# Optimization experiments

Measured on AMD Instinct MI355X. Metric: run time of the kernel, lower is better.

Reference implementation:

```python
import jax, jax.numpy as jnp
import numpy as np

NEG_SLOPE = 0.2
HEADS = 8

def _gat_conv(x, src, dst, n_nodes, W, att_src, att_dst, bias):
    # x: [N, Fin], W: [Fin, H*C], att_*: [H, C], bias: [C]
    H, C = att_src.shape
    xl = (x @ W).reshape(n_nodes, H, C)                      # [N,H,C]
    a_src = (xl * att_src[None]).sum(-1)                      # [N,H]
    a_dst = (xl * att_dst[None]).sum(-1)                      # [N,H]
    e = jax.nn.leaky_relu(a_src[src] + a_dst[dst], NEG_SLOPE) # [E,H]
    m = jax.ops.segment_max(e, dst, num_segments=n_nodes)     # [N,H]
    ee = jnp.exp(e - m[dst])
    s = jax.ops.segment_sum(ee, dst, num_segments=n_nodes)    # [N,H]
    alpha = ee / s[dst]                                       # [E,H]
    msg = alpha[:, :, None] * xl[src]                         # [E,H,C]
    out = jax.ops.segment_sum(msg, dst, num_segments=n_nodes) # [N,H,C]
    return out.mean(axis=1) + bias                            # [N,C] (concat=False)

def setup_inputs() -> dict:
    key = jax.random.key(0)
    ks = jax.random.split(key, 12)
    N, E, EL = 50000, 800000, 200000
    V, D, HID, OUT = 5000, 128, 32, 32
    inp = {}
    inp['x'] = jax.random.randint(ks[0], (N,), 0, V)
    inp['edge_index'] = jax.random.randint(ks[1], (2, E), 0, N)
    inp['edge_label_index'] = jax.random.randint(ks[2], (2, EL), 0, N)
    inp['emb'] = jax.random.normal(ks[3], (V, D), jnp.float32) * D ** -0.5
    inp['W1'] = jax.random.normal(ks[4], (D, HEADS * HID), jnp.float32) * D ** -0.5
    inp['att_src1'] = jax.random.normal(ks[5], (HEADS, HID), jnp.float32) * HID ** -0.5
    inp['att_dst1'] = jax.random.normal(ks[6], (HEADS, HID), jnp.float32) * HID ** -0.5
    inp['b1'] = jnp.zeros((HID,), jnp.float32)
    inp['W2'] = jax.random.normal(ks[7], (HID, HEADS * OUT), jnp.float32) * HID ** -0.5
    inp['att_src2'] = jax.random.normal(ks[8], (HEADS, OUT), jnp.float32) * OUT ** -0.5
    inp['att_dst2'] = jax.random.normal(ks[9], (HEADS, OUT), jnp.float32) * OUT ** -0.5
    inp['b2'] = jnp.zeros((OUT,), jnp.float32)
    return inp

def reference(x, edge_index, edge_label_index, emb, W1, att_src1, att_dst1, b1, W2, att_src2, att_dst2, b2):
    N = x.shape[0]
    # PyG GATConv adds self-loops by default
    loop = jnp.arange(N)
    src = jnp.concatenate([edge_index[0], loop])
    dst = jnp.concatenate([edge_index[1], loop])
    h = emb[x]                                                   # [N, D] embedding lookup (squeeze(1) equivalent)
    h = jax.nn.relu(_gat_conv(h, src, dst, N, W1, att_src1, att_dst1, b1))
    # dropout p=0.5 is identity at inference (training=False)
    z = _gat_conv(h, src, dst, N, W2, att_src2, att_dst2, b2)    # [N, OUT]
    # decode: dot product over label edges
    return (z[edge_label_index[0]] * z[edge_label_index[1]]).sum(axis=-1)
```

## Files before the change

### kernel.cpp

```cpp
#include <hip/hip_runtime.h>
#include <hip/hip_fp16.h>
#include <math.h>
#include <limits.h>

#define HH 8
#define CC 32
#define NEG 0.2f

struct __align__(8) half4 { __half2 a, b; };
typedef float f32x4 __attribute__((ext_vector_type(4)));

__device__ __forceinline__ int ldnt(const int* p){ return __builtin_nontemporal_load(p); }
__device__ __forceinline__ float ldntf(const float* p){ return __builtin_nontemporal_load(p); }
__device__ __forceinline__ f32x4 ldnt4(const float* p){ return __builtin_nontemporal_load((const f32x4*)p); }
__device__ __forceinline__ void stnt4(float* p, f32x4 v){ __builtin_nontemporal_store(v, (f32x4*)p); }
__device__ __forceinline__ int f2ord(float f){ int i=__float_as_int(f); return i>=0? i : i^0x7fffffff; }
__device__ __forceinline__ float ord2f(int i){ return __int_as_float(i>=0? i : i^0x7fffffff); }

__device__ __forceinline__ void edge_sd_nt(const int* __restrict__ ei, int e, int E, int& s, int& d){
  if(e < E){ s = ldnt(ei+e); d = ldnt(ei+E+e); } else { s = e-E; d = s; }
}

__global__ void k_init2(int* __restrict__ cnt, int* __restrict__ gmax, int N){
  int i = blockIdx.x*blockDim.x + threadIdx.x;
  if(i < N) cnt[i] = 0;
  if(i < 16) gmax[i] = INT_MIN;
}

__global__ void k_count(const int* __restrict__ ei, int E, int ET, int* __restrict__ cnt){
  int e = blockIdx.x*blockDim.x + threadIdx.x;
  if(e >= ET) return;
  int d = (e < E) ? ldnt(ei+E+e) : e-E;
  atomicAdd(&cnt[d], 1);
}

__global__ __launch_bounds__(256) void k_scan_block(const int* __restrict__ cnt,
                                                    int* __restrict__ off,
                                                    int* __restrict__ bsum, int N){
  int i = blockIdx.x*256 + threadIdx.x;
  int v = (i < N) ? cnt[i] : 0;
  int lane = threadIdx.x & 63;
  int incl = v;
  #pragma unroll
  for(int o=1;o<64;o<<=1){ int u = __shfl_up(incl,o); if(lane>=o) incl += u; }
  __shared__ int wsum[4];
  if(lane==63) wsum[threadIdx.x>>6] = incl;
  __syncthreads();
  int w = threadIdx.x>>6, wadd = 0;
  #pragma unroll
  for(int k=0;k<4;k++) if(k<w) wadd += wsum[k];
  if(i < N) off[i] = wadd + incl - v;
  if(threadIdx.x==255) bsum[blockIdx.x] = wadd + incl;
}

__global__ __launch_bounds__(256) void k_scan_bsum(int* __restrict__ bsum, int nb,
                                                   int* __restrict__ offN){
  int t = threadIdx.x;
  int v = (t < nb) ? bsum[t] : 0;
  int lane = t & 63;
  int incl = v;
  #pragma unroll
  for(int o=1;o<64;o<<=1){ int u = __shfl_up(incl,o); if(lane>=o) incl += u; }
  __shared__ int wsum[4];
  if(lane==63) wsum[t>>6] = incl;
  __syncthreads();
  int w = t>>6, wadd = 0;
  #pragma unroll
  for(int k=0;k<4;k++) if(k<w) wadd += wsum[k];
  if(t < nb) bsum[t] = wadd + incl - v;
  if(t == 255) *offN = wadd + incl;
}

__global__ void k_scan_add(int* __restrict__ off, const int* __restrict__ bsum,
                           int* __restrict__ cur, int N){
  int i = blockIdx.x*256 + threadIdx.x;
  if(i < N){ int v = off[i] + bsum[blockIdx.x]; off[i] = v; cur[i] = v; }
}

__global__ void k_scatter(const int* __restrict__ ei, int E, int ET,
                          const int* __restrict__ x,
                          int* __restrict__ cur, int* __restrict__ csr_src,
                          int* __restrict__ csr_xv){
  int e = blockIdx.x*blockDim.x + threadIdx.x;
  if(e >= ET) return;
  int s,d; edge_sd_nt(ei,e,E,s,d);
  int pos = atomicAdd(&cur[d], 1);
  csr_src[pos] = s;
  csr_xv[pos]  = x[s];
}

__global__ __launch_bounds__(256) void k_ws(const float* __restrict__ W2,
                                            const float* __restrict__ att_s2,
                                            const float* __restrict__ att_d2,
                                            float* __restrict__ ws_s, float* __restrict__ ws_d){
  int k = threadIdx.x >> 3, h = threadIdx.x & 7;
  float ss = 0.f, dd = 0.f;
  for(int c=0;c<CC;c++){
    float w = W2[k*256 + h*CC + c];
    ss = fmaf(w, att_s2[h*CC+c], ss);
    dd = fmaf(w, att_d2[h*CC+c], dd);
  }
  ws_s[k*HH+h] = ss;
  ws_d[k*HH+h] = dd;
}

__global__ __launch_bounds__(256) void k_gmax(const float* __restrict__ a, int n8,
                                              int* __restrict__ gmax){
  int tid = blockIdx.x*256 + threadIdx.x;
  int lane = threadIdx.x & 63;
  float m = -INFINITY;
  for(int i = tid; i < n8; i += gridDim.x*256) m = fmaxf(m, a[i]);
  #pragma unroll
  for(int msk=8; msk<64; msk<<=1) m = fmaxf(m, __shfl_xor(m, msk));
  if(lane < 8) atomicMax(&gmax[lane], f2ord(m));
}

__global__ __launch_bounds__(256,4) void k_gemm1(
    const float* __restrict__ X, const float* __restrict__ W,
    const float* __restrict__ att_s, const float* __restrict__ att_d,
    __half* __restrict__ xl, float* __restrict__ a_src, float* __restrict__ a_dst,
    int* __restrict__ gmax1, int V){
  const int ROWS = 8, FIN = 128;
  __shared__ __align__(16) float xs[ROWS][FIN];
  __shared__ int smax[8];
  int row0 = blockIdx.x*ROWS;
  int tid = threadIdx.x;
  if(tid < 8) smax[tid] = INT_MIN;
  for(int p = tid; p < ROWS*FIN; p += 256){
    int r = p/FIN, kk = p - r*FIN;
    int row = row0 + r;
    xs[r][kk] = (row < V) ? ldntf(X + (size_t)row*FIN + kk) : 0.f;
  }
  __syncthreads();
  float acc[ROWS];
  #pragma unroll
  for(int r=0;r<ROWS;r++) acc[r]=0.f;
  for(int k=0;k<FIN;k++){
    float w = W[(size_t)k*256 + tid];
    #pragma unroll
    for(int r=0;r<ROWS;r++) acc[r] = fmaf(xs[r][k], w, acc[r]);
  }
  float as = att_s[tid], ad = att_d[tid];
  #pragma unroll
  for(int r=0;r<ROWS;r++){
    int n = row0+r;
    float v = acc[r];
    float ps = v*as, pd = v*ad;
    #pragma unroll
    for(int msk=16; msk>=1; msk>>=1){
      ps += __shfl_xor(ps, msk);
      pd += __shfl_xor(pd, msk);
    }
    if(n < V){
      xl[(size_t)n*256 + tid] = __float2half(v);
      if((tid&31)==0){
        int hh = tid>>5;
        a_src[n*HH+hh] = ps;
        a_dst[n*HH+hh] = pd;
        atomicMax(&smax[hh], f2ord(ps));
      }
    }
  }
  __syncthreads();
  if(tid < 8) atomicMax(&gmax1[tid], smax[tid]);
}

__global__ __launch_bounds__(256) void k_fused1(
    const int* __restrict__ off, const int* __restrict__ csr_xv,
    const int* __restrict__ x,
    const float* __restrict__ a_src_v, const float* __restrict__ a_dst_v,
    const int* __restrict__ gmax1,
    const __half* __restrict__ xl_v, const float* __restrict__ bias,
    const float* __restrict__ ws_s, const float* __restrict__ ws_d,
    __half* __restrict__ h2h, float* __restrict__ a_src2, float* __restrict__ a_dst2, int N){
  int wid = (int)((blockIdx.x*(size_t)blockDim.x + threadIdx.x) >> 6);
  int lane = threadIdx.x & 63;
  if(wid >= N) return;
  const int start = off[wid], end = off[wid+1];
  const int t = lane >> 3, h = lane & 7;
  const int xv_n = x[wid];
  const float ad = a_dst_v[xv_n*HH + h];
  float mb = ord2f(gmax1[h]) + ad;
  mb = mb > 0.f ? mb : NEG*mb;

  const int h2 = lane >> 3, c0 = (lane & 7)*4;
  const __half* xp = xl_v + h2*CC + c0;

  int sv = ldnt(csr_xv + min(start + t, end-1));
  float sraw = a_src_v[sv*HH + h] + ad;
  bool valid = (start + t) < end;

  float eesum = 0.f;
  float4 acc = make_float4(0.f,0.f,0.f,0.f);
  for(int j0 = start; j0 < end; j0 += 8){
    int svn = 0; float srawn = 0.f; bool validn = false;
    if(j0 + 8 < end){
      int jjn = j0 + 8 + t;
      svn = ldnt(csr_xv + min(jjn, end-1));
      srawn = a_src_v[svn*HH + h] + ad;
      validn = jjn < end;
    }
    float v = sraw > 0.f ? sraw : NEG*sraw;
    float ee = valid ? __expf(v - mb) : 0.f;
    eesum += ee;
    float av[8];
    #pragma unroll
    for(int u=0;u<8;u++) av[u] = __shfl(ee, u*8 + h2);
    int s0 = __builtin_amdgcn_readlane(sv, 0);
    int s1 = __builtin_amdgcn_readlane(sv, 8);
    int s2 = __builtin_amdgcn_readlane(sv, 16);
    int s3 = __builtin_amdgcn_readlane(sv, 24);
    int s4 = __builtin_amdgcn_readlane(sv, 32);
    int s5 = __builtin_amdgcn_readlane(sv, 40);
    int s6 = __builtin_amdgcn_readlane(sv, 48);
    int s7 = __builtin_amdgcn_readlane(sv, 56);
    uint2 rv[8];
    rv[0] = *reinterpret_cast<const uint2*>(xp + (size_t)s0*256);
    rv[1] = *reinterpret_cast<const uint2*>(xp + (size_t)s1*256);
    rv[2] = *reinterpret_cast<const uint2*>(xp + (size_t)s2*256);
    rv[3] = *reinterpret_cast<const uint2*>(xp + (size_t)s3*256);
    rv[4] = *reinterpret_cast<const uint2*>(xp + (size_t)s4*256);
    rv[5] = *reinterpret_cast<const uint2*>(xp + (size_t)s5*256);
    rv[6] = *reinterpret_cast<const uint2*>(xp + (size_t)s6*256);
    rv[7] = *reinterpret_cast<const uint2*>(xp + (size_t)s7*256);
    #pragma unroll
    for(int u=0;u<8;u++){
      __half2 ha = *reinterpret_cast<__half2*>(&rv[u].x);
      __half2 hb = *reinterpret_cast<__half2*>(&rv[u].y);
      float2 f01 = __half22float2(ha), f23 = __half22float2(hb);
      acc.x = fmaf(av[u], f01.x, acc.x);
      acc.y = fmaf(av[u], f01.y, acc.y);
      acc.z = fmaf(av[u], f23.x, acc.z);
      acc.w = fmaf(av[u], f23.y, acc.w);
    }
    sv = svn; sraw = srawn; valid = validn;
  }
  #pragma unroll
  for(int msk=8; msk<64; msk<<=1) eesum += __shfl_xor(eesum, msk);
  float is2 = 0.125f / __shfl(eesum, h2);
  acc.x *= is2; acc.y *= is2; acc.z *= is2; acc.w *= is2;
  #pragma unroll
  for(int msk=8; msk<64; msk<<=1){
    acc.x += __shfl_xor(acc.x, msk);
    acc.y += __shfl_xor(acc.y, msk);
    acc.z += __shfl_xor(acc.z, msk);
    acc.w += __shfl_xor(acc.w, msk);
  }
  if(lane < 8){
    const float4 b = *reinterpret_cast<const float4*>(bias + c0);
    float4 o = make_float4(fmaxf(acc.x+b.x,0.f), fmaxf(acc.y+b.y,0.f),
                           fmaxf(acc.z+b.z,0.f), fmaxf(acc.w+b.w,0.f));
    half4 hv;
    hv.a = __floats2half2_rn(o.x, o.y);
    hv.b = __floats2half2_rn(o.z, o.w);
    *reinterpret_cast<half4*>(h2h + (size_t)wid*CC + c0) = hv;
    float ps = 0.f, pd = 0.f;
    #pragma unroll
    for(int g=0; g<8; ++g){
      float v0 = __shfl(o.x, g), v1 = __shfl(o.y, g), v2 = __shfl(o.z, g), v3 = __shfl(o.w, g);
      int kb = g*4;
      ps = fmaf(v0, ws_s[(kb+0)*HH+lane], ps);
      ps = fmaf(v1, ws_s[(kb+1)*HH+lane], ps);
      ps = fmaf(v2, ws_s[(kb+2)*HH+lane], ps);
      ps = fmaf(v3, ws_s[(kb+3)*HH+lane], ps);
      pd = fmaf(v0, ws_d[(kb+0)*HH+lane], pd);
      pd = fmaf(v1, ws_d[(kb+1)*HH+lane], pd);
      pd = fmaf(v2, ws_d[(kb+2)*HH+lane], pd);
      pd = fmaf(v3, ws_d[(kb+3)*HH+lane], pd);
    }
    a_src2[wid*HH + lane] = ps;
    a_dst2[wid*HH + lane] = pd;
  }
}

__global__ __launch_bounds__(256) void k_agg2(
    const int* __restrict__ off, const int* __restrict__ csr_src,
    const float* __restrict__ a_src2, const float* __restrict__ a_dst2,
    const int* __restrict__ gmax2,
    const __half* __restrict__ h2h, float* __restrict__ agg, int N){
  int wid = (int)((blockIdx.x*(size_t)blockDim.x + threadIdx.x) >> 6);
  int lane = threadIdx.x & 63;
  if(wid >= N) return;
  const int start = off[wid], end = off[wid+1];
  const int t = lane >> 3, h = lane & 7;
  const float ad = a_dst2[wid*HH + h];
  float mb = ord2f(gmax2[h]) + ad;
  mb = mb > 0.f ? mb : NEG*mb;

  const int h2 = lane >> 3, k0 = (lane & 7)*4;
  const __half* hp = h2h + k0;

  int sv = ldnt(csr_src + min(start + t, end-1));
  float sraw = a_src2[sv*HH + h] + ad;
  bool valid = (start + t) < end;

  float eesum = 0.f;
  float4 acc = make_float4(0.f,0.f,0.f,0.f);
  for(int j0 = start; j0 < end; j0 += 8){
    int svn = 0; float srawn = 0.f; bool validn = false;
    if(j0 + 8 < end){
      int jjn = j0 + 8 + t;
      svn = ldnt(csr_src + min(jjn, end-1));
      srawn = a_src2[svn*HH + h] + ad;
      validn = jjn < end;
    }
    float v = sraw > 0.f ? sraw : NEG*sraw;
    float ee = valid ? __expf(v - mb) : 0.f;
    eesum += ee;
    float av[8];
    #pragma unroll
    for(int u=0;u<8;u++) av[u] = __shfl(ee, u*8 + h2);
    int s0 = __builtin_amdgcn_readlane(sv, 0);
    int s1 = __builtin_amdgcn_readlane(sv, 8);
    int s2 = __builtin_amdgcn_readlane(sv, 16);
    int s3 = __builtin_amdgcn_readlane(sv, 24);
    int s4 = __builtin_amdgcn_readlane(sv, 32);
    int s5 = __builtin_amdgcn_readlane(sv, 40);
    int s6 = __builtin_amdgcn_readlane(sv, 48);
    int s7 = __builtin_amdgcn_readlane(sv, 56);
    uint2 rv[8];
    rv[0] = *reinterpret_cast<const uint2*>(hp + (size_t)s0*CC);
    rv[1] = *reinterpret_cast<const uint2*>(hp + (size_t)s1*CC);
    rv[2] = *reinterpret_cast<const uint2*>(hp + (size_t)s2*CC);
    rv[3] = *reinterpret_cast<const uint2*>(hp + (size_t)s3*CC);
    rv[4] = *reinterpret_cast<const uint2*>(hp + (size_t)s4*CC);
    rv[5] = *reinterpret_cast<const uint2*>(hp + (size_t)s5*CC);
    rv[6] = *reinterpret_cast<const uint2*>(hp + (size_t)s6*CC);
    rv[7] = *reinterpret_cast<const uint2*>(hp + (size_t)s7*CC);
    #pragma unroll
    for(int u=0;u<8;u++){
      __half2 ha = *reinterpret_cast<__half2*>(&rv[u].x);
      __half2 hb = *reinterpret_cast<__half2*>(&rv[u].y);
      float2 f01 = __half22float2(ha), f23 = __half22float2(hb);
      acc.x = fmaf(av[u], f01.x, acc.x);
      acc.y = fmaf(av[u], f01.y, acc.y);
      acc.z = fmaf(av[u], f23.x, acc.z);
      acc.w = fmaf(av[u], f23.y, acc.w);
    }
    sv = svn; sraw = srawn; valid = validn;
  }
  #pragma unroll
  for(int msk=8; msk<64; msk<<=1) eesum += __shfl_xor(eesum, msk);
  float is2 = 0.125f / __shfl(eesum, h2);
  f32x4 o; o.x = acc.x*is2; o.y = acc.y*is2; o.z = acc.z*is2; o.w = acc.w*is2;
  stnt4(agg + (size_t)wid*256 + lane*4, o);
}

__global__ __launch_bounds__(256) void k_trans2(
    const float* __restrict__ agg, const float* __restrict__ W2,
    const float* __restrict__ b2, float* __restrict__ z, int N){
  __shared__ __align__(16) float aggl[4][256];
  int w = threadIdx.x >> 6, lane = threadIdx.x & 63;
  int wid = (int)(blockIdx.x*4 + w);
  bool active = wid < N;
  f32x4 av = {0.f,0.f,0.f,0.f};
  if(active) av = ldnt4(agg + (size_t)wid*256 + lane*4);
  *reinterpret_cast<f32x4*>(&aggl[w][lane*4]) = av;
  __syncthreads();

  const int ch = lane & 31, part = lane >> 5;
  float p0=0.f, p1=0.f, p2=0.f, p3=0.f;
  #pragma unroll
  for(int hh = 0; hh < 4; ++hh){
    int hq = part*4 + hh;
    const float* wcol = W2 + hq*CC + ch;
    const float* a = &aggl[w][hq*CC];
    #pragma unroll
    for(int k=0;k<CC;k+=4){
      p0 = fmaf(a[k+0], wcol[(size_t)(k+0)*256], p0);
      p1 = fmaf(a[k+1], wcol[(size_t)(k+1)*256], p1);
      p2 = fmaf(a[k+2], wcol[(size_t)(k+2)*256], p2);
      p3 = fmaf(a[k+3], wcol[(size_t)(k+3)*256], p3);
    }
  }
  float p = (p0+p1)+(p2+p3);
  p += __shfl_xor(p, 32);
  if(active && part==0) z[(size_t)wid*CC + ch] = p + b2[ch];
}

__global__ void k_decode(const int* __restrict__ eli, int EL,
                         const float* __restrict__ z, float* __restrict__ out){
  int e = blockIdx.x*blockDim.x + threadIdx.x;
  if(e >= EL) return;
  const float4* za = reinterpret_cast<const float4*>(z + (size_t)ldnt(eli+e)*CC);
  const float4* zb = reinterpret_cast<const float4*>(z + (size_t)ldnt(eli+EL+e)*CC);
  float s = 0.f;
  #pragma unroll
  for(int j=0;j<8;j++){
    float4 u = za[j], v = zb[j];
    s += u.x*v.x + u.y*v.y + u.z*v.z + u.w*v.w;
  }
  out[e] = s;
}

extern "C" void kernel_launch(void* const* d_in, const int* in_sizes, int n_in,
                              void* d_out, int out_size, void* d_ws, size_t ws_size,
                              hipStream_t stream){
  const int*   x   = (const int*)d_in[0];
  const int*   ei  = (const int*)d_in[1];
  const int*   eli = (const int*)d_in[2];
  const float* emb = (const float*)d_in[3];
  const float* W1  = (const float*)d_in[4];
  const float* as1 = (const float*)d_in[5];
  const float* ad1 = (const float*)d_in[6];
  const float* b1  = (const float*)d_in[7];
  const float* W2  = (const float*)d_in[8];
  const float* as2 = (const float*)d_in[9];
  const float* ad2 = (const float*)d_in[10];
  const float* b2  = (const float*)d_in[11];

  const int N  = in_sizes[0];
  const int V  = in_sizes[3]/128;
  const int E  = in_sizes[1]/2;
  const int EL = in_sizes[2]/2;
  const int ET = E + N;

  __half* xl_v = (__half*)d_ws;
  __half* h2h  = xl_v + (size_t)V*256;
  float* a_src_v = (float*)(h2h + (size_t)N*CC);
  float* a_dst_v = a_src_v + (size_t)V*HH;
  float* a_src2  = a_dst_v + (size_t)V*HH;
  float* a_dst2  = a_src2 + (size_t)N*HH;
  float* z       = a_dst2 + (size_t)N*HH;
  float* agg     = z + (size_t)N*CC;
  float* ws_s    = agg + (size_t)N*256;
  float* ws_d    = ws_s + 256;
  int*   gmax1   = (int*)(ws_d + 256);
  int*   gmax2   = gmax1 + 8;
  int*   cnt   = gmax2 + 8;
  int*   off   = cnt + N;
  int*   cur   = off + N + 1;
  int*   bsum  = cur + N;
  int*   csr   = bsum + ((N+255)/256);
  int*   csr_xv= csr + ET;

  dim3 blk(256);
  auto cdiv = [](long long a, long long b){ return (unsigned)((a+b-1)/b); };
  const int nb = (int)cdiv(N,256);

  k_init2<<<cdiv(N,256), blk, 0, stream>>>(cnt, gmax1, N);
  k_count<<<cdiv(ET,256), blk, 0, stream>>>(ei, E, ET, cnt);
  k_scan_block<<<nb, blk, 0, stream>>>(cnt, off, bsum, N);
  k_scan_bsum<<<1, blk, 0, stream>>>(bsum, nb, off + N);
  k_scan_add<<<nb, blk, 0, stream>>>(off, bsum, cur, N);
  k_scatter<<<cdiv(ET,256), blk, 0, stream>>>(ei, E, ET, x, cur, csr, csr_xv);

  k_ws<<<1, blk, 0, stream>>>(W2, as2, ad2, ws_s, ws_d);

  k_gemm1<<<cdiv(V,8), blk, 0, stream>>>(emb, W1, as1, ad1, xl_v, a_src_v, a_dst_v, gmax1, V);
  k_fused1<<<cdiv((long long)N*64,256), blk, 0, stream>>>(off, csr_xv, x, a_src_v, a_dst_v,
                                                          gmax1, xl_v, b1, ws_s, ws_d,
                                                          h2h, a_src2, a_dst2, N);

  k_gmax<<<64, blk, 0, stream>>>(a_src2, N*HH, gmax2);
  k_agg2<<<cdiv((long long)N*64,256), blk, 0, stream>>>(off, csr, a_src2, a_dst2,
                                                        gmax2, h2h, agg, N);
  k_trans2<<<cdiv(N,4), blk, 0, stream>>>(agg, W2, b2, z, N);

  k_decode<<<cdiv(EL,256), blk, 0, stream>>>(eli, EL, z, (float*)d_out);
}
```

Measured before the change: 327.9 us.

## Fuse layer-2 aggregation with projection and fold global max into fused1

Merges the layer-2 attention aggregation kernel with the W2 projection kernel, so each wavefront's 256-wide aggregate goes into shared memory instead of through a global N×256 float buffer. The separate gmax reduction kernel is removed: fused1 now computes a per-block max of a_src2 in shared memory and writes it with one atomic per head. The a_src2/a_dst2 dot products are spread across all 64 lanes with xor-shuffle reductions instead of running serially in 8 lanes. Together these cut about 51 MB of global write and read traffic and two kernel launches, at the cost of more register pressure in the fused kernel.

```diff
diff --git a/kernel.cpp b/kernel.cpp
--- a/kernel.cpp
+++ b/kernel.cpp
@@ -12,8 +12,6 @@
 
 __device__ __forceinline__ int ldnt(const int* p){ return __builtin_nontemporal_load(p); }
 __device__ __forceinline__ float ldntf(const float* p){ return __builtin_nontemporal_load(p); }
-__device__ __forceinline__ f32x4 ldnt4(const float* p){ return __builtin_nontemporal_load((const f32x4*)p); }
-__device__ __forceinline__ void stnt4(float* p, f32x4 v){ __builtin_nontemporal_store(v, (f32x4*)p); }
 __device__ __forceinline__ int f2ord(float f){ int i=__float_as_int(f); return i>=0? i : i^0x7fffffff; }
 __device__ __forceinline__ float ord2f(int i){ return __int_as_float(i>=0? i : i^0x7fffffff); }
 
@@ -102,17 +100,6 @@
   }
   ws_s[k*HH+h] = ss;
   ws_d[k*HH+h] = dd;
-}
-
-__global__ __launch_bounds__(256) void k_gmax(const float* __restrict__ a, int n8,
-                                              int* __restrict__ gmax){
-  int tid = blockIdx.x*256 + threadIdx.x;
-  int lane = threadIdx.x & 63;
-  float m = -INFINITY;
-  for(int i = tid; i < n8; i += gridDim.x*256) m = fmaxf(m, a[i]);
-  #pragma unroll
-  for(int msk=8; msk<64; msk<<=1) m = fmaxf(m, __shfl_xor(m, msk));
-  if(lane < 8) atomicMax(&gmax[lane], f2ord(m));
 }
 
 __global__ __launch_bounds__(256,4) void k_gemm1(
@@ -172,190 +159,196 @@
     const int* __restrict__ gmax1,
     const __half* __restrict__ xl_v, const float* __restrict__ bias,
     const float* __restrict__ ws_s, const float* __restrict__ ws_d,
-    __half* __restrict__ h2h, float* __restrict__ a_src2, float* __restrict__ a_dst2, int N){
+    __half* __restrict__ h2h, float* __restrict__ a_src2, float* __restrict__ a_dst2,
+    int* __restrict__ gmax2, int N){
+  __shared__ int smax[8];
   int wid = (int)((blockIdx.x*(size_t)blockDim.x + threadIdx.x) >> 6);
   int lane = threadIdx.x & 63;
-  if(wid >= N) return;
-  const int start = off[wid], end = off[wid+1];
-  const int t = lane >> 3, h = lane & 7;
-  const int xv_n = x[wid];
-  const float ad = a_dst_v[xv_n*HH + h];
-  float mb = ord2f(gmax1[h]) + ad;
-  mb = mb > 0.f ? mb : NEG*mb;
-
-  const int h2 = lane >> 3, c0 = (lane & 7)*4;
-  const __half* xp = xl_v + h2*CC + c0;
-
-  int sv = ldnt(csr_xv + min(start + t, end-1));
-  float sraw = a_src_v[sv*HH + h] + ad;
-  bool valid = (start + t) < end;
-
-  float eesum = 0.f;
-  float4 acc = make_float4(0.f,0.f,0.f,0.f);
-  for(int j0 = start; j0 < end; j0 += 8){
-    int svn = 0; float srawn = 0.f; bool validn = false;
-    if(j0 + 8 < end){
-      int jjn = j0 + 8 + t;
-      svn = ldnt(csr_xv + min(jjn, end-1));
-      srawn = a_src_v[svn*HH + h] + ad;
-      validn = jjn < end;
-    }
-    float v = sraw > 0.f ? sraw : NEG*sraw;
-    float ee = valid ? __expf(v - mb) : 0.f;
-    eesum += ee;
-    float av[8];
-    #pragma unroll
-    for(int u=0;u<8;u++) av[u] = __shfl(ee, u*8 + h2);
-    int s0 = __builtin_amdgcn_readlane(sv, 0);
-    int s1 = __builtin_amdgcn_readlane(sv, 8);
-    int s2 = __builtin_amdgcn_readlane(sv, 16);
-    int s3 = __builtin_amdgcn_readlane(sv, 24);
-    int s4 = __builtin_amdgcn_readlane(sv, 32);
-    int s5 = __builtin_amdgcn_readlane(sv, 40);
-    int s6 = __builtin_amdgcn_readlane(sv, 48);
-    int s7 = __builtin_amdgcn_readlane(sv, 56);
-    uint2 rv[8];
-    rv[0] = *reinterpret_cast<const uint2*>(xp + (size_t)s0*256);
-    rv[1] = *reinterpret_cast<const uint2*>(xp + (size_t)s1*256);
-    rv[2] = *reinterpret_cast<const uint2*>(xp + (size_t)s2*256);
-    rv[3] = *reinterpret_cast<const uint2*>(xp + (size_t)s3*256);
-    rv[4] = *reinterpret_cast<const uint2*>(xp + (size_t)s4*256);
-    rv[5] = *reinterpret_cast<const uint2*>(xp + (size_t)s5*256);
-    rv[6] = *reinterpret_cast<const uint2*>(xp + (size_t)s6*256);
-    rv[7] = *reinterpret_cast<const uint2*>(xp + (size_t)s7*256);
-    #pragma unroll
-    for(int u=0;u<8;u++){
-      __half2 ha = *reinterpret_cast<__half2*>(&rv[u].x);
-      __half2 hb = *reinterpret_cast<__half2*>(&rv[u].y);
-      float2 f01 = __half22float2(ha), f23 = __half22float2(hb);
-      acc.x = fmaf(av[u], f01.x, acc.x);
-      acc.y = fmaf(av[u], f01.y, acc.y);
-      acc.z = fmaf(av[u], f23.x, acc.z);
-      acc.w = fmaf(av[u], f23.y, acc.w);
-    }
-    sv = svn; sraw = srawn; valid = validn;
-  }
-  #pragma unroll
-  for(int msk=8; msk<64; msk<<=1) eesum += __shfl_xor(eesum, msk);
-  float is2 = 0.125f / __shfl(eesum, h2);
-  acc.x *= is2; acc.y *= is2; acc.z *= is2; acc.w *= is2;
-  #pragma unroll
-  for(int msk=8; msk<64; msk<<=1){
-    acc.x += __shfl_xor(acc.x, msk);
-    acc.y += __shfl_xor(acc.y, msk);
-    acc.z += __shfl_xor(acc.z, msk);
-    acc.w += __shfl_xor(acc.w, msk);
-  }
-  if(lane < 8){
+  if(threadIdx.x < 8) smax[threadIdx.x] = INT_MIN;
+  __syncthreads();
+  const bool act = wid < N;
+  const int h2 = lane >> 3, q = lane & 7, c0 = q*4;
+
+  if(act){
+    const int start = off[wid], end = off[wid+1];
+    const int t = lane >> 3, h = lane & 7;
+    const int xv_n = x[wid];
+    const float ad = a_dst_v[xv_n*HH + h];
+    float mb = ord2f(gmax1[h]) + ad;
+    mb = mb > 0.f ? mb : NEG*mb;
+
+    const __half* xp = xl_v + h2*CC + c0;
+
+    int sv = ldnt(csr_xv + min(start + t, end-1));
+    float sraw = a_src_v[sv*HH + h] + ad;
+    bool valid = (start + t) < end;
+
+    float eesum = 0.f;
+    float4 acc = make_float4(0.f,0.f,0.f,0.f);
+    for(int j0 = start; j0 < end; j0 += 8){
+      int svn = 0; float srawn = 0.f; bool validn = false;
+      if(j0 + 8 < end){
+        int jjn = j0 + 8 + t;
+        svn = ldnt(csr_xv + min(jjn, end-1));
+        srawn = a_src_v[svn*HH + h] + ad;
+        validn = jjn < end;
+      }
+      float v = sraw > 0.f ? sraw : NEG*sraw;
+      float ee = valid ? __expf(v - mb) : 0.f;
+      eesum += ee;
+      float av[8];
+      #pragma unroll
+      for(int u=0;u<8;u++) av[u] = __shfl(ee, u*8 + h2);
+      int s0 = __builtin_amdgcn_readlane(sv, 0);
+      int s1 = __builtin_amdgcn_readlane(sv, 8);
+      int s2 = __builtin_amdgcn_readlane(sv, 16);
+      int s3 = __builtin_amdgcn_readlane(sv, 24);
+      int s4 = __builtin_amdgcn_readlane(sv, 32);
+      int s5 = __builtin_amdgcn_readlane(sv, 40);
+      int s6 = __builtin_amdgcn_readlane(sv, 48);
+      int s7 = __builtin_amdgcn_readlane(sv, 56);
+      uint2 rv[8];
+      rv[0] = *reinterpret_cast<const uint2*>(xp + (size_t)s0*256);
+      rv[1] = *reinterpret_cast<const uint2*>(xp + (size_t)s1*256);
+      rv[2] = *reinterpret_cast<const uint2*>(xp + (size_t)s2*256);
+      rv[3] = *reinterpret_cast<const uint2*>(xp + (size_t)s3*256);
+      rv[4] = *reinterpret_cast<const uint2*>(xp + (size_t)s4*256);
+      rv[5] = *reinterpret_cast<const uint2*>(xp + (size_t)s5*256);
+      rv[6] = *reinterpret_cast<const uint2*>(xp + (size_t)s6*256);
+      rv[7] = *reinterpret_cast<const uint2*>(xp + (size_t)s7*256);
+      #pragma unroll
+      for(int u=0;u<8;u++){
+        __half2 ha = *reinterpret_cast<__half2*>(&rv[u].x);
+        __half2 hb = *reinterpret_cast<__half2*>(&rv[u].y);
+        float2 f01 = __half22float2(ha), f23 = __half22float2(hb);
+        acc.x = fmaf(av[u], f01.x, acc.x);
+        acc.y = fmaf(av[u], f01.y, acc.y);
+        acc.z = fmaf(av[u], f23.x, acc.z);
+        acc.w = fmaf(av[u], f23.y, acc.w);
+      }
+      sv = svn; sraw = srawn; valid = validn;
+    }
+    #pragma unroll
+    for(int msk=8; msk<64; msk<<=1) eesum += __shfl_xor(eesum, msk);
+    float is2 = 0.125f / __shfl(eesum, h2);
+    acc.x *= is2; acc.y *= is2; acc.z *= is2; acc.w *= is2;
+    #pragma unroll
+    for(int msk=8; msk<64; msk<<=1){
+      acc.x += __shfl_xor(acc.x, msk);
+      acc.y += __shfl_xor(acc.y, msk);
+      acc.z += __shfl_xor(acc.z, msk);
+      acc.w += __shfl_xor(acc.w, msk);
+    }
     const float4 b = *reinterpret_cast<const float4*>(bias + c0);
     float4 o = make_float4(fmaxf(acc.x+b.x,0.f), fmaxf(acc.y+b.y,0.f),
                            fmaxf(acc.z+b.z,0.f), fmaxf(acc.w+b.w,0.f));
-    half4 hv;
-    hv.a = __floats2half2_rn(o.x, o.y);
-    hv.b = __floats2half2_rn(o.z, o.w);
-    *reinterpret_cast<half4*>(h2h + (size_t)wid*CC + c0) = hv;
+    if(lane < 8){
+      half4 hv;
+      hv.a = __floats2half2_rn(o.x, o.y);
+      hv.b = __floats2half2_rn(o.z, o.w);
+      *reinterpret_cast<half4*>(h2h + (size_t)wid*CC + c0) = hv;
+    }
     float ps = 0.f, pd = 0.f;
-    #pragma unroll
-    for(int g=0; g<8; ++g){
-      float v0 = __shfl(o.x, g), v1 = __shfl(o.y, g), v2 = __shfl(o.z, g), v3 = __shfl(o.w, g);
-      int kb = g*4;
-      ps = fmaf(v0, ws_s[(kb+0)*HH+lane], ps);
-      ps = fmaf(v1, ws_s[(kb+1)*HH+lane], ps);
-      ps = fmaf(v2, ws_s[(kb+2)*HH+lane], ps);
-      ps = fmaf(v3, ws_s[(kb+3)*HH+lane], ps);
-      pd = fmaf(v0, ws_d[(kb+0)*HH+lane], pd);
-      pd = fmaf(v1, ws_d[(kb+1)*HH+lane], pd);
-      pd = fmaf(v2, ws_d[(kb+2)*HH+lane], pd);
-      pd = fmaf(v3, ws_d[(kb+3)*HH+lane], pd);
-    }
-    a_src2[wid*HH + lane] = ps;
-    a_dst2[wid*HH + lane] = pd;
-  }
-}
-
-__global__ __launch_bounds__(256) void k_agg2(
+    ps = fmaf(o.x, ws_s[(4*q+0)*HH + h2], ps);
+    ps = fmaf(o.y, ws_s[(4*q+1)*HH + h2], ps);
+    ps = fmaf(o.z, ws_s[(4*q+2)*HH + h2], ps);
+    ps = fmaf(o.w, ws_s[(4*q+3)*HH + h2], ps);
+    pd = fmaf(o.x, ws_d[(4*q+0)*HH + h2], pd);
+    pd = fmaf(o.y, ws_d[(4*q+1)*HH + h2], pd);
+    pd = fmaf(o.z, ws_d[(4*q+2)*HH + h2], pd);
+    pd = fmaf(o.w, ws_d[(4*q+3)*HH + h2], pd);
+    #pragma unroll
+    for(int msk=1; msk<8; msk<<=1){
+      ps += __shfl_xor(ps, msk);
+      pd += __shfl_xor(pd, msk);
+    }
+    if(q == 0){
+      a_src2[wid*HH + h2] = ps;
+      a_dst2[wid*HH + h2] = pd;
+      atomicMax(&smax[h2], f2ord(ps));
+    }
+  }
+  __syncthreads();
+  if(threadIdx.x < 8) atomicMax(&gmax2[threadIdx.x], smax[threadIdx.x]);
+}
+
+__global__ __launch_bounds__(256) void k_fused2(
     const int* __restrict__ off, const int* __restrict__ csr_src,
     const float* __restrict__ a_src2, const float* __restrict__ a_dst2,
     const int* __restrict__ gmax2,
-    const __half* __restrict__ h2h, float* __restrict__ agg, int N){
-  int wid = (int)((blockIdx.x*(size_t)blockDim.x + threadIdx.x) >> 6);
-  int lane = threadIdx.x & 63;
-  if(wid >= N) return;
-  const int start = off[wid], end = off[wid+1];
-  const int t = lane >> 3, h = lane & 7;
-  const float ad = a_dst2[wid*HH + h];
-  float mb = ord2f(gmax2[h]) + ad;
-  mb = mb > 0.f ? mb : NEG*mb;
-
-  const int h2 = lane >> 3, k0 = (lane & 7)*4;
-  const __half* hp = h2h + k0;
-
-  int sv = ldnt(csr_src + min(start + t, end-1));
-  float sraw = a_src2[sv*HH + h] + ad;
-  bool valid = (start + t) < end;
-
-  float eesum = 0.f;
-  float4 acc = make_float4(0.f,0.f,0.f,0.f);
-  for(int j0 = start; j0 < end; j0 += 8){
-    int svn = 0; float srawn = 0.f; bool validn = false;
-    if(j0 + 8 < end){
-      int jjn = j0 + 8 + t;
-      svn = ldnt(csr_src + min(jjn, end-1));
-      srawn = a_src2[svn*HH + h] + ad;
-      validn = jjn < end;
-    }
-    float v = sraw > 0.f ? sraw : NEG*sraw;
-    float ee = valid ? __expf(v - mb) : 0.f;
-    eesum += ee;
-    float av[8];
-    #pragma unroll
-    for(int u=0;u<8;u++) av[u] = __shfl(ee, u*8 + h2);
-    int s0 = __builtin_amdgcn_readlane(sv, 0);
-    int s1 = __builtin_amdgcn_readlane(sv, 8);
-    int s2 = __builtin_amdgcn_readlane(sv, 16);
-    int s3 = __builtin_amdgcn_readlane(sv, 24);
-    int s4 = __builtin_amdgcn_readlane(sv, 32);
-    int s5 = __builtin_amdgcn_readlane(sv, 40);
-    int s6 = __builtin_amdgcn_readlane(sv, 48);
-    int s7 = __builtin_amdgcn_readlane(sv, 56);
-    uint2 rv[8];
-    rv[0] = *reinterpret_cast<const uint2*>(hp + (size_t)s0*CC);
-    rv[1] = *reinterpret_cast<const uint2*>(hp + (size_t)s1*CC);
-    rv[2] = *reinterpret_cast<const uint2*>(hp + (size_t)s2*CC);
-    rv[3] = *reinterpret_cast<const uint2*>(hp + (size_t)s3*CC);
-    rv[4] = *reinterpret_cast<const uint2*>(hp + (size_t)s4*CC);
-    rv[5] = *reinterpret_cast<const uint2*>(hp + (size_t)s5*CC);
-    rv[6] = *reinterpret_cast<const uint2*>(hp + (size_t)s6*CC);
-    rv[7] = *reinterpret_cast<const uint2*>(hp + (size_t)s7*CC);
-    #pragma unroll
-    for(int u=0;u<8;u++){
-      __half2 ha = *reinterpret_cast<__half2*>(&rv[u].x);
-      __half2 hb = *reinterpret_cast<__half2*>(&rv[u].y);
-      float2 f01 = __half22float2(ha), f23 = __half22float2(hb);
-      acc.x = fmaf(av[u], f01.x, acc.x);
-      acc.y = fmaf(av[u], f01.y, acc.y);
-      acc.z = fmaf(av[u], f23.x, acc.z);
-      acc.w = fmaf(av[u], f23.y, acc.w);
-    }
-    sv = svn; sraw = srawn; valid = validn;
-  }
-  #pragma unroll
-  for(int msk=8; msk<64; msk<<=1) eesum += __shfl_xor(eesum, msk);
-  float is2 = 0.125f / __shfl(eesum, h2);
-  f32x4 o; o.x = acc.x*is2; o.y = acc.y*is2; o.z = acc.z*is2; o.w = acc.w*is2;
-  stnt4(agg + (size_t)wid*256 + lane*4, o);
-}
-
-__global__ __launch_bounds__(256) void k_trans2(
-    const float* __restrict__ agg, const float* __restrict__ W2,
+    const __half* __restrict__ h2h, const float* __restrict__ W2,
     const float* __restrict__ b2, float* __restrict__ z, int N){
   __shared__ __align__(16) float aggl[4][256];
   int w = threadIdx.x >> 6, lane = threadIdx.x & 63;
   int wid = (int)(blockIdx.x*4 + w);
-  bool active = wid < N;
-  f32x4 av = {0.f,0.f,0.f,0.f};
-  if(active) av = ldnt4(agg + (size_t)wid*256 + lane*4);
-  *reinterpret_cast<f32x4*>(&aggl[w][lane*4]) = av;
+  const bool act = wid < N;
+  const int h2 = lane >> 3, k0 = (lane & 7)*4;
+  f32x4 oo = {0.f,0.f,0.f,0.f};
+
+  if(act){
+    const int start = off[wid], end = off[wid+1];
+    const int t = lane >> 3, h = lane & 7;
+    const float ad = a_dst2[wid*HH + h];
+    float mb = ord2f(gmax2[h]) + ad;
+    mb = mb > 0.f ? mb : NEG*mb;
+
+    const __half* hp = h2h + k0;
+
+    int sv = ldnt(csr_src + min(start + t, end-1));
+    float sraw = a_src2[sv*HH + h] + ad;
+    bool valid = (start + t) < end;
+
+    float eesum = 0.f;
+    float4 acc = make_float4(0.f,0.f,0.f,0.f);
+    for(int j0 = start; j0 < end; j0 += 8){
+      int svn = 0; float srawn = 0.f; bool validn = false;
+      if(j0 + 8 < end){
+        int jjn = j0 + 8 + t;
+        svn = ldnt(csr_src + min(jjn, end-1));
+        srawn = a_src2[svn*HH + h] + ad;
+        validn = jjn < end;
+      }
+      float v = sraw > 0.f ? sraw : NEG*sraw;
+      float ee = valid ? __expf(v - mb) : 0.f;
+      eesum += ee;
+      float av[8];
+      #pragma unroll
+      for(int u=0;u<8;u++) av[u] = __shfl(ee, u*8 + h2);
+      int s0 = __builtin_amdgcn_readlane(sv, 0);
+      int s1 = __builtin_amdgcn_readlane(sv, 8);
+      int s2 = __builtin_amdgcn_readlane(sv, 16);
+      int s3 = __builtin_amdgcn_readlane(sv, 24);
+      int s4 = __builtin_amdgcn_readlane(sv, 32);
+      int s5 = __builtin_amdgcn_readlane(sv, 40);
+      int s6 = __builtin_amdgcn_readlane(sv, 48);
+      int s7 = __builtin_amdgcn_readlane(sv, 56);
+      uint2 rv[8];
+      rv[0] = *reinterpret_cast<const uint2*>(hp + (size_t)s0*CC);
+      rv[1] = *reinterpret_cast<const uint2*>(hp + (size_t)s1*CC);
+      rv[2] = *reinterpret_cast<const uint2*>(hp + (size_t)s2*CC);
+      rv[3] = *reinterpret_cast<const uint2*>(hp + (size_t)s3*CC);
+      rv[4] = *reinterpret_cast<const uint2*>(hp + (size_t)s4*CC);
+      rv[5] = *reinterpret_cast<const uint2*>(hp + (size_t)s5*CC);
+      rv[6] = *reinterpret_cast<const uint2*>(hp + (size_t)s6*CC);
+      rv[7] = *reinterpret_cast<const uint2*>(hp + (size_t)s7*CC);
+      #pragma unroll
+      for(int u=0;u<8;u++){
+        __half2 ha = *reinterpret_cast<__half2*>(&rv[u].x);
+        __half2 hb = *reinterpret_cast<__half2*>(&rv[u].y);
+        float2 f01 = __half22float2(ha), f23 = __half22float2(hb);
+        acc.x = fmaf(av[u], f01.x, acc.x);
+        acc.y = fmaf(av[u], f01.y, acc.y);
+        acc.z = fmaf(av[u], f23.x, acc.z);
+        acc.w = fmaf(av[u], f23.y, acc.w);
+      }
+      sv = svn; sraw = srawn; valid = validn;
+    }
+    #pragma unroll
+    for(int msk=8; msk<64; msk<<=1) eesum += __shfl_xor(eesum, msk);
+    float is2 = 0.125f / __shfl(eesum, h2);
+    oo.x = acc.x*is2; oo.y = acc.y*is2; oo.z = acc.z*is2; oo.w = acc.w*is2;
+  }
+  *reinterpret_cast<f32x4*>(&aggl[w][h2*CC + k0]) = oo;
   __syncthreads();
 
   const int ch = lane & 31, part = lane >> 5;
@@ -375,7 +368,7 @@
   }
   float p = (p0+p1)+(p2+p3);
   p += __shfl_xor(p, 32);
-  if(active && part==0) z[(size_t)wid*CC + ch] = p + b2[ch];
+  if(act && part==0) z[(size_t)wid*CC + ch] = p + b2[ch];
 }
 
 __global__ void k_decode(const int* __restrict__ eli, int EL,
@@ -422,8 +415,7 @@
   float* a_src2  = a_dst_v + (size_t)V*HH;
   float* a_dst2  = a_src2 + (size_t)N*HH;
   float* z       = a_dst2 + (size_t)N*HH;
-  float* agg     = z + (size_t)N*CC;
-  float* ws_s    = agg + (size_t)N*256;
+  float* ws_s    = z + (size_t)N*CC;
   float* ws_d    = ws_s + 256;
   int*   gmax1   = (int*)(ws_d + 256);
   int*   gmax2   = gmax1 + 8;
@@ -450,12 +442,10 @@
   k_gemm1<<<cdiv(V,8), blk, 0, stream>>>(emb, W1, as1, ad1, xl_v, a_src_v, a_dst_v, gmax1, V);
   k_fused1<<<cdiv((long long)N*64,256), blk, 0, stream>>>(off, csr_xv, x, a_src_v, a_dst_v,
                                                           gmax1, xl_v, b1, ws_s, ws_d,
-                                                          h2h, a_src2, a_dst2, N);
-
-  k_gmax<<<64, blk, 0, stream>>>(a_src2, N*HH, gmax2);
-  k_agg2<<<cdiv((long long)N*64,256), blk, 0, stream>>>(off, csr, a_src2, a_dst2,
-                                                        gmax2, h2h, agg, N);
-  k_trans2<<<cdiv(N,4), blk, 0, stream>>>(agg, W2, b2, z, N);
+                                                          h2h, a_src2, a_dst2, gmax2, N);
+
+  k_fused2<<<cdiv(N,4), blk, 0, stream>>>(off, csr, a_src2, a_dst2,
+                                          gmax2, h2h, W2, b2, z, N);
 
   k_decode<<<cdiv(EL,256), blk, 0, stream>>>(eli, EL, z, (float*)d_out);
 }
```

Measured after the change: 969.1 us. 2.96x slower.
